# Kernel tuning notes

Hardware: AMD Instinct MI355X
Metric: run time of the kernel (lower is better)

## Reference

```python
import jax, jax.numpy as jnp
import numpy as np

B, W, N = 4, 8, 1024
F_IN, HID, OUT = 256, 256, 128


def setup_inputs() -> dict:
    key = jax.random.key(0)
    ks = jax.random.split(key, 8)
    X = jax.random.normal(ks[0], (B, W, N, F_IN), dtype=jnp.float32)
    adj = jax.random.uniform(ks[1], (B, W, N, N), dtype=jnp.float32)
    # Linear params, torch default init: U(-1/sqrt(fan_in), 1/sqrt(fan_in))
    def lin(k, fi, fo):
        k1, k2 = jax.random.split(k)
        bnd = 1.0 / np.sqrt(fi)
        Wm = jax.random.uniform(k1, (fi, fo), minval=-bnd, maxval=bnd, dtype=jnp.float32)
        bm = jax.random.uniform(k2, (fo,), minval=-bnd, maxval=bnd, dtype=jnp.float32)
        return Wm, bm
    W1, b1 = lin(ks[2], F_IN, HID)
    W2, b2 = lin(ks[3], HID, HID)
    W3, b3 = lin(ks[4], HID, OUT)
    return {"X": X, "adj": adj, "W1": W1, "b1": b1, "W2": W2, "b2": b2, "W3": W3, "b3": b3}


def _normalize(adj):
    # adj: [B, W, N, N]. adj_hat = adj + I; sym degree norm D^-1/2 A D^-1/2
    n = adj.shape[-1]
    adj_hat = adj + jnp.eye(n, dtype=adj.dtype)
    d = jnp.sum(adj_hat, axis=-1) ** (-0.5)            # [B, W, N]
    # diag(d) @ adj_hat @ diag(d) == row/col scaling (same math, no N^3 diag matmuls)
    return adj_hat * d[..., :, None] * d[..., None, :]


def reference(X, adj, W1, b1, W2, b2, W3, b3):
    adj_norm = _normalize(adj)                          # [B, W, N, N]
    h = X
    for Wm, bm in ((W1, b1), (W2, b2), (W3, b3)):
        h = jnp.einsum('bwnm,bwmf->bwnf', adj_norm, h)  # aggregate
        h = jax.nn.relu(jnp.einsum('bwnf,fo->bwno', h, Wm) + bm)
    return h                                            # [B, W, N, OUT]
```

## Files before the change

kernel.cpp:

```cpp
#include <hip/hip_runtime.h>
#include <hip/hip_bf16.h>
#include <cstdint>
#include <cstddef>

#define NN 1024
#define FF 256

typedef __attribute__((ext_vector_type(8))) short bf16x8;
typedef __attribute__((ext_vector_type(4))) float f32x4;

__device__ __forceinline__ short f2bf(float x) {
  unsigned int u = __float_as_uint(x);
  u = (u + 0x7fffu + ((u >> 16) & 1u)) >> 16;
  return (short)u;
}


__global__ __launch_bounds__(256)
void dinv_cast(const float* __restrict__ adj, float* __restrict__ dinv,
               short* __restrict__ Ahat) {
  __shared__ float wsum[64];
  int b = blockIdx.x;
  int bw = b >> 6, s = b & 63;
  int t = threadIdx.x;
  int wid = t >> 6, lane = t & 63;
  int row = lane & 15;
  int rloc = (s << 4) + row;
  int kg = (lane >> 4) & 3;
  const float* arow = adj + ((size_t)(bw << 10) + rloc) * NN;
  short* outb = Ahat + ((size_t)bw << 20) + ((size_t)s << 14) + (t << 3);
  float ssum = 0.f;
  #pragma unroll
  for (int it = 0; it < 8; it++) {
    int col = (it << 7) + (wid << 5) + (kg << 3);
    float4 a0 = *(const float4*)(arow + col);
    float4 a1 = *(const float4*)(arow + col + 4);
    float v[8] = {a0.x, a0.y, a0.z, a0.w, a1.x, a1.y, a1.z, a1.w};
    union { ushort o[8]; int4 q; } pk;
    #pragma unroll
    for (int j = 0; j < 8; j++) {
      v[j] += (rloc == col + j) ? 1.f : 0.f;
      ssum += v[j];
      pk.o[j] = (ushort)f2bf(v[j]);
    }
    *(int4*)(outb + (it << 11)) = pk.q;
  }
  ssum += __shfl_down(ssum, 32, 64);
  ssum += __shfl_down(ssum, 16, 64);
  if (lane < 16) wsum[(wid << 4) + lane] = ssum;
  __syncthreads();
  if (t < 16) {
    float tot = wsum[t] + wsum[16 + t] + wsum[32 + t] + wsum[48 + t];
    dinv[(bw << 10) + (s << 4) + t] = rsqrtf(tot);
  }
}

__global__ __launch_bounds__(256)
void transpose_x(const float* __restrict__ X, const float* __restrict__ dinv,
                 short* __restrict__ XT) {
  __shared__ short T[64][72];
  int bwo = blockIdx.z;
  int n0 = blockIdx.x << 6, f0 = blockIdx.y << 6;
  int t = threadIdx.x;
  {
    int n = t >> 2, fc = (t & 3) << 4;
    float dn = dinv[(bwo << 10) + n0 + n];
    const float* src = X + (((size_t)bwo * NN + n0 + n) * FF) + f0 + fc;
    #pragma unroll
    for (int i = 0; i < 4; i++) {
      float4 v = ((const float4*)src)[i];
      ushort4 p;
      p.x = (unsigned short)f2bf(v.x * dn); p.y = (unsigned short)f2bf(v.y * dn);
      p.z = (unsigned short)f2bf(v.z * dn); p.w = (unsigned short)f2bf(v.w * dn);
      *(ushort4*)&T[n][fc + (i << 2)] = p;
    }
  }
  __syncthreads();
  {
    int f = t >> 2, nc = (t & 3) << 4;
    int fg = f0 + f, ng = n0 + nc;
    short tmp[16];
    #pragma unroll
    for (int i = 0; i < 16; i++) tmp[i] = T[nc + i][f];
    size_t e0 = ((size_t)bwo << 18) + ((size_t)(fg >> 4) << 14) + ((ng >> 5) << 9)
              + (((ng & 31) >> 3) << 7) + ((fg & 15) << 3);
    *(int4*)(XT + e0)       = *(int4*)&tmp[0];
    *(int4*)(XT + e0 + 128) = *(int4*)&tmp[8];
  }
}

__global__ __launch_bounds__(256)
void transpose_w(const float* __restrict__ W, short* __restrict__ WT, int FO) {
  int idx = blockIdx.x * 256 + threadIdx.x;
  if (idx >= FO * 256) return;
  int fo = idx >> 8, fi = idx & 255;
  size_t e = (size_t)((fo >> 4) << 12) + ((fi >> 5) << 9)
           + (((fi & 31) >> 3) << 7) + ((fo & 15) << 3) + (fi & 7);
  WT[e] = f2bf(W[fi * FO + fo]);
}

template<int F_OUT, bool FINAL>
__global__ __launch_bounds__(512, 4)
void gcn_layer(const short* __restrict__ Ahat,
               const float* __restrict__ dinv,
               const short* __restrict__ Gin,
               const short* __restrict__ WT,
               const float* __restrict__ bias,
               short* __restrict__ Gout,
               float* __restrict__ Out) {
  __shared__ short aggL[64 * 272];

  int b = blockIdx.x;
  int bw = ((b & 7) << 2) + ((b >> 3) & 3);
  int rb = b >> 5;
  int r0 = rb << 6;

  int tid = threadIdx.x;
  int wid = tid >> 6, lane = tid & 63;
  int l15 = lane & 15, l4 = lane >> 4;
  int wr = wid >> 2, wf = wid & 3;

  const short* Hbase = Gin  + ((size_t)bw << 18) + ((size_t)(wf << 2) << 14) + (lane << 3);
  const short* Abase = Ahat + ((size_t)bw << 20)
                     + ((size_t)((rb << 2) + (wr << 1)) << 14) + (lane << 3);
  const float* dvB = dinv + (bw << 10);
  float dsc0 = dvB[r0 + (wr << 5) + l15];
  float dsc1 = dvB[r0 + (wr << 5) + 16 + l15];

  f32x4 acc[4][2];
  #pragma unroll
  for (int am = 0; am < 4; am++)
    #pragma unroll
    for (int nf = 0; nf < 2; nf++) acc[am][nf] = f32x4{0.f, 0.f, 0.f, 0.f};

  bf16x8 he[4], ae[2], ho[4], ao[2];

#define LD(HB, AB, T)                                                         \
  {                                                                           \
    _Pragma("unroll")                                                         \
    for (int am = 0; am < 4; am++)                                            \
      HB[am] = *(const bf16x8*)(Hbase + am * 16384 + (T) * 512);              \
    _Pragma("unroll")                                                         \
    for (int nf = 0; nf < 2; nf++)                                            \
      AB[nf] = *(const bf16x8*)(Abase + nf * 16384 + (T) * 512);              \
  }
#define MM(HB, AB)                                                            \
  _Pragma("unroll")                                                           \
  for (int am = 0; am < 4; am++)                                              \
    _Pragma("unroll")                                                         \
    for (int nf = 0; nf < 2; nf++)                                            \
      acc[am][nf] = __builtin_amdgcn_mfma_f32_16x16x32_bf16(                  \
          HB[am], AB[nf], acc[am][nf], 0, 0, 0);

  LD(he, ae, 0);
  LD(ho, ao, 1);
  #pragma unroll
  for (int it = 0; it < 16; ++it) {
    MM(he, ae);
    if (it < 15) LD(he, ae, 2 * it + 2);
    MM(ho, ao);
    if (it < 15) LD(ho, ao, 2 * it + 3);
  }
#undef LD
#undef MM

  #pragma unroll
  for (int am = 0; am < 4; am++)
    #pragma unroll
    for (int nf = 0; nf < 2; nf++) {
      int r = (wr << 5) + (nf << 4) + l15;
      float ds = nf ? dsc1 : dsc0;
      int fB = ((wf << 6) + (am << 4) + (l4 << 2)) << 1;
      int off = (r * 544 + (fB ^ ((r & 7) << 4))) >> 1;
      ushort4 p;
      p.x = (unsigned short)f2bf(acc[am][nf][0] * ds);
      p.y = (unsigned short)f2bf(acc[am][nf][1] * ds);
      p.z = (unsigned short)f2bf(acc[am][nf][2] * ds);
      p.w = (unsigned short)f2bf(acc[am][nf][3] * ds);
      *(ushort4*)(aggL + off) = p;
    }
  __syncthreads();

  constexpr int NFO = F_OUT / 64;
  const short* Wbase = WT + (size_t)(wf * NFO) * 4096 + (lane << 3);
  f32x4 acc2[2][NFO];
  #pragma unroll
  for (int am = 0; am < 2; am++)
    #pragma unroll
    for (int nf = 0; nf < NFO; nf++) acc2[am][nf] = f32x4{0.f, 0.f, 0.f, 0.f};

  #pragma unroll
  for (int kt = 0; kt < 8; kt++) {
    bf16x8 af[2];
    #pragma unroll
    for (int am = 0; am < 2; am++) {
      int r = (wr << 5) + (am << 4) + l15;
      int fB = (kt << 6) + (l4 << 4);
      af[am] = *(const bf16x8*)(aggL + ((r * 544 + (fB ^ ((r & 7) << 4))) >> 1));
    }
    #pragma unroll
    for (int nf = 0; nf < NFO; nf++) {
      bf16x8 wv = *(const bf16x8*)(Wbase + (size_t)nf * 4096 + (kt << 9));
      #pragma unroll
      for (int am = 0; am < 2; am++)
        acc2[am][nf] = __builtin_amdgcn_mfma_f32_16x16x32_bf16(af[am], wv, acc2[am][nf], 0, 0, 0);
    }
  }

  #pragma unroll
  for (int am = 0; am < 2; am++) {
    int nodeLoc = (wr << 5) + (am << 4) + (l4 << 2);
    float4 dn4 = *(const float4*)(dvB + r0 + nodeLoc);
    float dn[4] = {dn4.x, dn4.y, dn4.z, dn4.w};
    #pragma unroll
    for (int nf = 0; nf < NFO; nf++) {
      int fo = wf * (F_OUT / 4) + (nf << 4) + l15;
      float bb = bias[fo];
      float v[4];
      #pragma unroll
      for (int j = 0; j < 4; j++) v[j] = fmaxf(acc2[am][nf][j] + bb, 0.f);
      if (!FINAL) {
        ushort4 p;
        p.x = (unsigned short)f2bf(v[0] * dn[0]);
        p.y = (unsigned short)f2bf(v[1] * dn[1]);
        p.z = (unsigned short)f2bf(v[2] * dn[2]);
        p.w = (unsigned short)f2bf(v[3] * dn[3]);
        size_t e = (size_t)bw * (F_OUT * 1024) + ((size_t)(fo >> 4) << 14)
                 + ((size_t)((rb << 1) + wr) << 9)
                 + ((size_t)((am << 1) + (l4 >> 1)) << 7)
                 + ((fo & 15) << 3) + ((l4 & 1) << 2);
        *(ushort4*)(Gout + e) = p;
      } else {
        float* ob = Out + ((size_t)(bw << 10) + r0 + nodeLoc) * F_OUT + fo;
        ob[0]         = v[0];
        ob[F_OUT]     = v[1];
        ob[2 * F_OUT] = v[2];
        ob[3 * F_OUT] = v[3];
      }
    }
  }
}

extern "C" void kernel_launch(void* const* d_in, const int* in_sizes, int n_in,
                              void* d_out, int out_size, void* d_ws, size_t ws_size,
                              hipStream_t stream) {
  const float* X   = (const float*)d_in[0];
  const float* adj = (const float*)d_in[1];
  const float* W1  = (const float*)d_in[2];
  const float* b1  = (const float*)d_in[3];
  const float* W2  = (const float*)d_in[4];
  const float* b2  = (const float*)d_in[5];
  const float* W3  = (const float*)d_in[6];
  const float* b3  = (const float*)d_in[7];
  float* out = (float*)d_out;

  char* ws = (char*)d_ws;
  float* dinv = (float*)ws;
  short* WT1  = (short*)(ws + 131072);
  short* WT2  = (short*)(ws + 262144);
  short* WT3  = (short*)(ws + 393216);
  short* bufA = (short*)(ws + 458752);
  short* bufB = (short*)(ws + 458752 + 16777216);
  short* Ahat = (short*)(ws + 458752 + 2 * 16777216);

  dinv_cast<<<2048, 256, 0, stream>>>(adj, dinv, Ahat);
  transpose_x<<<dim3(16, 4, 32), 256, 0, stream>>>(X, dinv, bufA);
  transpose_w<<<256, 256, 0, stream>>>(W1, WT1, 256);
  transpose_w<<<256, 256, 0, stream>>>(W2, WT2, 256);
  transpose_w<<<128, 256, 0, stream>>>(W3, WT3, 128);

  gcn_layer<256, false><<<512, 512, 0, stream>>>(Ahat, dinv, bufA, WT1, b1, bufB, nullptr);
  gcn_layer<256, false><<<512, 512, 0, stream>>>(Ahat, dinv, bufB, WT2, b2, bufA, nullptr);
  gcn_layer<128, true ><<<512, 512, 0, stream>>>(Ahat, dinv, bufA, WT3, b3, nullptr, out);
}
```

Before: 161.3 us.

## Use 4-wave blocks with larger per-wave aggregation tiles and MFMA priority

Each gcn_layer block drops from 8 waves to 4, so every wave now covers all 64 rows of the block (a 64x64 output tile per wave instead of 32x64). Each loaded H fragment is reused across four A fragments, which halves redundant H loads per block and raises the MFMA-to-load ratio. The block-to-(bw,rb) mapping is reordered and s_setprio brackets the MFMA bursts. The cost is more accumulator and fragment registers per wave (launch bounds become 256,3), which lowers the number of waves available to hide memory latency.

```diff
diff --git a/kernel.cpp b/kernel.cpp
--- a/kernel.cpp
+++ b/kernel.cpp
@@ -100,7 +100,7 @@
 }
 
 template<int F_OUT, bool FINAL>
-__global__ __launch_bounds__(512, 4)
+__global__ __launch_bounds__(256, 3)
 void gcn_layer(const short* __restrict__ Ahat,
                const float* __restrict__ dinv,
                const short* __restrict__ Gin,
@@ -111,90 +111,91 @@
   __shared__ short aggL[64 * 272];
 
   int b = blockIdx.x;
-  int bw = ((b & 7) << 2) + ((b >> 3) & 3);
-  int rb = b >> 5;
+  int x = b & 7, m = b >> 3;
+  int bw = (x << 2) + (m >> 4);
+  int rb = m & 15;
   int r0 = rb << 6;
 
   int tid = threadIdx.x;
-  int wid = tid >> 6, lane = tid & 63;
+  int wf = tid >> 6, lane = tid & 63;
   int l15 = lane & 15, l4 = lane >> 4;
-  int wr = wid >> 2, wf = wid & 3;
 
   const short* Hbase = Gin  + ((size_t)bw << 18) + ((size_t)(wf << 2) << 14) + (lane << 3);
-  const short* Abase = Ahat + ((size_t)bw << 20)
-                     + ((size_t)((rb << 2) + (wr << 1)) << 14) + (lane << 3);
+  const short* Abase = Ahat + ((size_t)bw << 20) + ((size_t)(rb << 2) << 14) + (lane << 3);
   const float* dvB = dinv + (bw << 10);
-  float dsc0 = dvB[r0 + (wr << 5) + l15];
-  float dsc1 = dvB[r0 + (wr << 5) + 16 + l15];
-
-  f32x4 acc[4][2];
-  #pragma unroll
-  for (int am = 0; am < 4; am++)
-    #pragma unroll
-    for (int nf = 0; nf < 2; nf++) acc[am][nf] = f32x4{0.f, 0.f, 0.f, 0.f};
-
-  bf16x8 he[4], ae[2], ho[4], ao[2];
+
+  f32x4 acc[4][4];
+  #pragma unroll
+  for (int ah = 0; ah < 4; ah++)
+    #pragma unroll
+    for (int aa = 0; aa < 4; aa++) acc[ah][aa] = f32x4{0.f, 0.f, 0.f, 0.f};
+
+  bf16x8 hE[4], aE[4], hO[4], aO[4];
 
 #define LD(HB, AB, T)                                                         \
   {                                                                           \
     _Pragma("unroll")                                                         \
-    for (int am = 0; am < 4; am++)                                            \
-      HB[am] = *(const bf16x8*)(Hbase + am * 16384 + (T) * 512);              \
+    for (int ah = 0; ah < 4; ah++)                                            \
+      HB[ah] = *(const bf16x8*)(Hbase + ah * 16384 + (T) * 512);              \
     _Pragma("unroll")                                                         \
-    for (int nf = 0; nf < 2; nf++)                                            \
-      AB[nf] = *(const bf16x8*)(Abase + nf * 16384 + (T) * 512);              \
+    for (int aa = 0; aa < 4; aa++)                                            \
+      AB[aa] = *(const bf16x8*)(Abase + aa * 16384 + (T) * 512);              \
   }
 #define MM(HB, AB)                                                            \
+  __builtin_amdgcn_s_setprio(1);                                              \
   _Pragma("unroll")                                                           \
-  for (int am = 0; am < 4; am++)                                              \
+  for (int ah = 0; ah < 4; ah++)                                              \
     _Pragma("unroll")                                                         \
-    for (int nf = 0; nf < 2; nf++)                                            \
-      acc[am][nf] = __builtin_amdgcn_mfma_f32_16x16x32_bf16(                  \
-          HB[am], AB[nf], acc[am][nf], 0, 0, 0);
-
-  LD(he, ae, 0);
-  LD(ho, ao, 1);
+    for (int aa = 0; aa < 4; aa++)                                            \
+      acc[ah][aa] = __builtin_amdgcn_mfma_f32_16x16x32_bf16(                  \
+          HB[ah], AB[aa], acc[ah][aa], 0, 0, 0);                              \
+  __builtin_amdgcn_s_setprio(0);
+
+  LD(hE, aE, 0);
+  LD(hO, aO, 1);
   #pragma unroll
   for (int it = 0; it < 16; ++it) {
-    MM(he, ae);
-    if (it < 15) LD(he, ae, 2 * it + 2);
-    MM(ho, ao);
-    if (it < 15) LD(ho, ao, 2 * it + 3);
+    MM(hE, aE);
+    if (it < 15) LD(hE, aE, 2 * it + 2);
+    MM(hO, aO);
+    if (it < 15) LD(hO, aO, 2 * it + 3);
   }
 #undef LD
 #undef MM
 
-  #pragma unroll
-  for (int am = 0; am < 4; am++)
-    #pragma unroll
-    for (int nf = 0; nf < 2; nf++) {
-      int r = (wr << 5) + (nf << 4) + l15;
-      float ds = nf ? dsc1 : dsc0;
-      int fB = ((wf << 6) + (am << 4) + (l4 << 2)) << 1;
+  float dsc[4];
+  #pragma unroll
+  for (int aa = 0; aa < 4; aa++) dsc[aa] = dvB[r0 + (aa << 4) + l15];
+  #pragma unroll
+  for (int ah = 0; ah < 4; ah++)
+    #pragma unroll
+    for (int aa = 0; aa < 4; aa++) {
+      int r = (aa << 4) + l15;
+      int fB = ((wf << 6) + (ah << 4) + (l4 << 2)) << 1;
       int off = (r * 544 + (fB ^ ((r & 7) << 4))) >> 1;
       ushort4 p;
-      p.x = (unsigned short)f2bf(acc[am][nf][0] * ds);
-      p.y = (unsigned short)f2bf(acc[am][nf][1] * ds);
-      p.z = (unsigned short)f2bf(acc[am][nf][2] * ds);
-      p.w = (unsigned short)f2bf(acc[am][nf][3] * ds);
+      p.x = (unsigned short)f2bf(acc[ah][aa][0] * dsc[aa]);
+      p.y = (unsigned short)f2bf(acc[ah][aa][1] * dsc[aa]);
+      p.z = (unsigned short)f2bf(acc[ah][aa][2] * dsc[aa]);
+      p.w = (unsigned short)f2bf(acc[ah][aa][3] * dsc[aa]);
       *(ushort4*)(aggL + off) = p;
     }
   __syncthreads();
 
   constexpr int NFO = F_OUT / 64;
   const short* Wbase = WT + (size_t)(wf * NFO) * 4096 + (lane << 3);
-  f32x4 acc2[2][NFO];
-  #pragma unroll
-  for (int am = 0; am < 2; am++)
+  f32x4 acc2[4][NFO];
+  #pragma unroll
+  for (int am = 0; am < 4; am++)
     #pragma unroll
     for (int nf = 0; nf < NFO; nf++) acc2[am][nf] = f32x4{0.f, 0.f, 0.f, 0.f};
 
   #pragma unroll
   for (int kt = 0; kt < 8; kt++) {
-    bf16x8 af[2];
-    #pragma unroll
-    for (int am = 0; am < 2; am++) {
-      int r = (wr << 5) + (am << 4) + l15;
+    bf16x8 af[4];
+    #pragma unroll
+    for (int am = 0; am < 4; am++) {
+      int r = (am << 4) + l15;
       int fB = (kt << 6) + (l4 << 4);
       af[am] = *(const bf16x8*)(aggL + ((r * 544 + (fB ^ ((r & 7) << 4))) >> 1));
     }
@@ -202,14 +203,14 @@
     for (int nf = 0; nf < NFO; nf++) {
       bf16x8 wv = *(const bf16x8*)(Wbase + (size_t)nf * 4096 + (kt << 9));
       #pragma unroll
-      for (int am = 0; am < 2; am++)
+      for (int am = 0; am < 4; am++)
         acc2[am][nf] = __builtin_amdgcn_mfma_f32_16x16x32_bf16(af[am], wv, acc2[am][nf], 0, 0, 0);
     }
   }
 
   #pragma unroll
-  for (int am = 0; am < 2; am++) {
-    int nodeLoc = (wr << 5) + (am << 4) + (l4 << 2);
+  for (int am = 0; am < 4; am++) {
+    int nodeLoc = (am << 4) + (l4 << 2);
     float4 dn4 = *(const float4*)(dvB + r0 + nodeLoc);
     float dn[4] = {dn4.x, dn4.y, dn4.z, dn4.w};
     #pragma unroll
@@ -226,8 +227,8 @@
         p.z = (unsigned short)f2bf(v[2] * dn[2]);
         p.w = (unsigned short)f2bf(v[3] * dn[3]);
         size_t e = (size_t)bw * (F_OUT * 1024) + ((size_t)(fo >> 4) << 14)
-                 + ((size_t)((rb << 1) + wr) << 9)
-                 + ((size_t)((am << 1) + (l4 >> 1)) << 7)
+                 + ((size_t)((rb << 1) + (am >> 1)) << 9)
+                 + ((size_t)(((am & 1) << 1) + (l4 >> 1)) << 7)
                  + ((fo & 15) << 3) + ((l4 & 1) << 2);
         *(ushort4*)(Gout + e) = p;
       } else {
@@ -269,7 +270,7 @@
   transpose_w<<<256, 256, 0, stream>>>(W2, WT2, 256);
   transpose_w<<<128, 256, 0, stream>>>(W3, WT3, 128);
 
-  gcn_layer<256, false><<<512, 512, 0, stream>>>(Ahat, dinv, bufA, WT1, b1, bufB, nullptr);
-  gcn_layer<256, false><<<512, 512, 0, stream>>>(Ahat, dinv, bufB, WT2, b2, bufA, nullptr);
-  gcn_layer<128, true ><<<512, 512, 0, stream>>>(Ahat, dinv, bufA, WT3, b3, nullptr, out);
-}
+  gcn_layer<256, false><<<512, 256, 0, stream>>>(Ahat, dinv, bufA, WT1, b1, bufB, nullptr);
+  gcn_layer<256, false><<<512, 256, 0, stream>>>(Ahat, dinv, bufB, WT2, b2, bufA, nullptr);
+  gcn_layer<128, true ><<<512, 256, 0, stream>>>(Ahat, dinv, bufA, WT3, b3, nullptr, out);
+}
```

Measured after the change: 138.9 us. -13.9%, faster.
